# Optimization experiments

Measured on AMD Instinct MI355X. Metric: run time of the kernel, lower is better.

The kernel has to match this reference:

```python
import jax, jax.numpy as jnp
import numpy as np

NT, C, B, N, H, E = 32768, 128, 64, 512, 4, 524288  # total nodes, channels, graphs, nodes/graph, heads, edges
DH = C // H
EPS = 1e-5


def batchnorm(x, g, b):
    # BatchNorm1d over the node dimension (training-mode batch statistics)
    m = x.mean(axis=0)
    v = x.var(axis=0)
    return (x - m) * jax.lax.rsqrt(v + EPS) * g + b


def setup_inputs() -> dict:
    key = jax.random.key(0)
    ks = jax.random.split(key, 8)
    s = 1.0 / np.sqrt(C)
    return dict(
        x=jax.random.normal(ks[0], (NT, C), jnp.float32),
        edge_index=jax.random.randint(ks[1], (2, E), 0, NT, dtype=jnp.int32),
        Wc=jax.random.normal(ks[2], (C, C), jnp.float32) * s,
        bc=jnp.zeros((C,), jnp.float32),
        in_proj_w=jax.random.normal(ks[3], (3 * C, C), jnp.float32) * s,
        in_proj_b=jnp.zeros((3 * C,), jnp.float32),
        out_proj_w=jax.random.normal(ks[4], (C, C), jnp.float32) * s,
        out_proj_b=jnp.zeros((C,), jnp.float32),
        gn1=jnp.ones((C,), jnp.float32), bn1=jnp.zeros((C,), jnp.float32),
        gn2=jnp.ones((C,), jnp.float32), bn2=jnp.zeros((C,), jnp.float32),
        gn3=jnp.ones((C,), jnp.float32), bn3=jnp.zeros((C,), jnp.float32),
        Wm1=jax.random.normal(ks[5], (2 * C, C), jnp.float32) * s,
        bm1=jnp.zeros((2 * C,), jnp.float32),
        Wm2=jax.random.normal(ks[6], (C, 2 * C), jnp.float32) / np.sqrt(2 * C),
        bm2=jnp.zeros((C,), jnp.float32),
    )


def reference(x, edge_index, Wc, bc, in_proj_w, in_proj_b, out_proj_w, out_proj_b,
              gn1, bn1, gn2, bn2, gn3, bn3, Wm1, bm1, Wm2, bm2):
    # --- local branch: mean-aggregation message passing + linear + residual + BN ---
    src, dst = edge_index[0], edge_index[1]
    agg = jax.ops.segment_sum(x[src], dst, num_segments=NT)            # [NT, C]
    cnt = jax.ops.segment_sum(jnp.ones((E, 1), x.dtype), dst, num_segments=NT)
    agg = agg / jnp.maximum(cnt, 1.0)
    h_local = agg @ Wc.T + bc + x                                       # dropout p=0 -> no-op
    h_local = batchnorm(h_local, gn1, bn1)

    # --- global branch: to_dense_batch (equal-size graphs -> reshape) + MHA ---
    hd = x.reshape(B, N, C)
    qkv = hd @ in_proj_w.T + in_proj_b                                  # [B, N, 3C]
    q, k, v = jnp.split(qkv, 3, axis=-1)
    q = q.reshape(B, N, H, DH).transpose(0, 2, 1, 3)                    # [B, H, N, DH]
    k = k.reshape(B, N, H, DH).transpose(0, 2, 1, 3)
    v = v.reshape(B, N, H, DH).transpose(0, 2, 1, 3)
    scores = jnp.einsum('bhqd,bhkd->bhqk', q, k) / np.sqrt(DH)          # [B, H, N, N]
    attn = jax.nn.softmax(scores, axis=-1)
    o = jnp.einsum('bhqk,bhkd->bhqd', attn, v)                          # [B, H, N, DH]
    o = o.transpose(0, 2, 1, 3).reshape(B, N, C)
    h_attn = (o @ out_proj_w.T + out_proj_b).reshape(NT, C) + x
    h_attn = batchnorm(h_attn, gn2, bn2)

    # --- combine + MLP + final norm ---
    out = h_local + h_attn
    out = out + (jax.nn.relu(out @ Wm1.T + bm1) @ Wm2.T + bm2)
    return batchnorm(out, gn3, bn3)
```

## Files before the change

### kernel.cpp

```cpp
#include <hip/hip_runtime.h>
#include <cstddef>

#define NT    32768
#define CCH   128
#define BB    64
#define NNODE 512
#define NHEAD 4
#define DHEAD 32
#define EE    524288
#define EPS   1e-5f
#define MAXDEG 96

typedef unsigned short u16;
typedef unsigned int   u32;
typedef __attribute__((ext_vector_type(8))) short short8;
typedef __attribute__((ext_vector_type(4))) short short4v;
typedef __attribute__((ext_vector_type(4))) float f32x4;

__device__ __forceinline__ float b2f(u32 w) { return __uint_as_float(w << 16); }
__device__ __forceinline__ u16 f2b(float f) {
    u32 u = __float_as_uint(f);
    u += 0x7FFF + ((u >> 16) & 1);
    return (u16)(u >> 16);
}

__global__ __launch_bounds__(256) void prep_kernel(const float* __restrict__ x,
                                                   const float* __restrict__ Wc,
                                                   const float* __restrict__ Wqkv,
                                                   const float* __restrict__ Wo,
                                                   const float* __restrict__ Wm1,
                                                   const float* __restrict__ Wm2,
                                                   u16* __restrict__ xb,
                                                   u16* __restrict__ Wcb,
                                                   u16* __restrict__ Wqkvb,
                                                   u16* __restrict__ Wob,
                                                   u16* __restrict__ Wm1b,
                                                   u16* __restrict__ Wm2b,
                                                   const int* __restrict__ ei,
                                                   int* __restrict__ cursor,
                                                   int* __restrict__ bucket) {
    if (blockIdx.x >= 2120) {
        int e = (blockIdx.x - 2120) * 256 + threadIdx.x;
        int src = ei[e];
        int dst = ei[EE + e];
        int pos = atomicAdd(cursor + dst, 1);
        if (pos < MAXDEG) bucket[dst * MAXDEG + pos] = src;
        return;
    }
    int r = blockIdx.x * 256 + threadIdx.x;
    const float* src; u16* dst;
    if (r < 524288) { src = x; dst = xb; }
    else if ((r -= 524288) < 2048) { src = Wc; dst = Wcb; }
    else if ((r -= 2048) < 6144) { src = Wqkv; dst = Wqkvb; }
    else if ((r -= 6144) < 2048) { src = Wo; dst = Wob; }
    else if ((r -= 2048) < 4096) { src = Wm1; dst = Wm1b; }
    else { r -= 4096; src = Wm2; dst = Wm2b; }
    size_t base = (size_t)r * 8;
    float4 a = *(const float4*)(src + base);
    float4 b = *(const float4*)(src + base + 4);
    uint4 u;
    u.x = (u32)f2b(a.x) | ((u32)f2b(a.y) << 16);
    u.y = (u32)f2b(a.z) | ((u32)f2b(a.w) << 16);
    u.z = (u32)f2b(b.x) | ((u32)f2b(b.y) << 16);
    u.w = (u32)f2b(b.z) | ((u32)f2b(b.w) << 16);
    *(uint4*)(dst + base) = u;
}

__global__ __launch_bounds__(256) void aggregate(const int* __restrict__ bucket,
                                                 const int* __restrict__ cursor,
                                                 const u16* __restrict__ xb,
                                                 u16* __restrict__ agg) {
    int ln = threadIdx.x >> 5;
    int c4 = threadIdx.x & 31;
    int n = blockIdx.x * 8 + ln;
    __shared__ int srcs[8][MAXDEG];
    int d = min(cursor[n], MAXDEG);
    for (int j = c4; j < d; j += 32) srcs[ln][j] = bucket[n * MAXDEG + j];
    __syncthreads();
    float s0 = 0.f, s1 = 0.f, s2 = 0.f, s3 = 0.f;
    for (int j = 0; j < d; ++j) {
        uint2 w = *(const uint2*)(xb + (size_t)srcs[ln][j] * CCH + c4 * 4);
        s0 += b2f(w.x & 0xffffu);
        s1 += b2f(w.x >> 16);
        s2 += b2f(w.y & 0xffffu);
        s3 += b2f(w.y >> 16);
    }
    float inv = 1.0f / fmaxf((float)d, 1.0f);
    uint2 out;
    out.x = (u32)f2b(s0 * inv) | ((u32)f2b(s1 * inv) << 16);
    out.y = (u32)f2b(s2 * inv) | ((u32)f2b(s3 * inv) << 16);
    *(uint2*)(agg + (size_t)n * CCH + c4 * 4) = out;
}

template <bool RELU, int RESID, bool STATS>
__global__ __launch_bounds__(256) void gemm_mfma(const u16* __restrict__ A,
                                                 const u16* __restrict__ W,
                                                 const float* __restrict__ bias,
                                                 const u16* __restrict__ residb,
                                                 u16* __restrict__ outb,
                                                 float* __restrict__ sum,
                                                 float* __restrict__ sumsq,
                                                 int M, int N, int K) {
    __shared__ u16 As[128 * 32];
    __shared__ u16 Bs[128 * 32];
    __shared__ u16 Cs[4][16 * 72];
    __shared__ float csum[128];
    __shared__ float csq[128];
    int m0 = blockIdx.x * 128, n0 = blockIdx.y * 128;
    int tid = threadIdx.x;
    int lane = tid & 63, wave = tid >> 6;
    int wm = (wave & 1) * 64, wn = (wave >> 1) * 64;
    int l15 = lane & 15, l4 = lane >> 4;

    if (STATS) {
        if (tid < 128) { csum[tid] = 0.f; csq[tid] = 0.f; }
    }

    f32x4 zero = {0.f, 0.f, 0.f, 0.f};
    f32x4 acc[4][4];
#pragma unroll
    for (int i = 0; i < 4; ++i)
#pragma unroll
        for (int j = 0; j < 4; ++j) acc[i][j] = zero;

    int srow = tid >> 2;
    int scol = (tid & 3) * 8;

    int kIter = K >> 5;
    uint4 a0 = *(const uint4*)(A + (size_t)(m0 + srow) * K + scol);
    uint4 a1 = *(const uint4*)(A + (size_t)(m0 + srow + 64) * K + scol);
    uint4 b0 = *(const uint4*)(W + (size_t)(n0 + srow) * K + scol);
    uint4 b1 = *(const uint4*)(W + (size_t)(n0 + srow + 64) * K + scol);
    for (int ki = 0; ki < kIter; ++ki) {
        if (ki) __syncthreads();
        *(uint4*)&As[srow * 32 + scol] = a0;
        *(uint4*)&As[(srow + 64) * 32 + scol] = a1;
        *(uint4*)&Bs[srow * 32 + scol] = b0;
        *(uint4*)&Bs[(srow + 64) * 32 + scol] = b1;
        if (ki + 1 < kIter) {
            int k0 = (ki + 1) * 32;
            a0 = *(const uint4*)(A + (size_t)(m0 + srow) * K + k0 + scol);
            a1 = *(const uint4*)(A + (size_t)(m0 + srow + 64) * K + k0 + scol);
            b0 = *(const uint4*)(W + (size_t)(n0 + srow) * K + k0 + scol);
            b1 = *(const uint4*)(W + (size_t)(n0 + srow + 64) * K + k0 + scol);
        }
        __syncthreads();
        short8 af[4], bf[4];
#pragma unroll
        for (int t = 0; t < 4; ++t) {
            af[t] = *(const short8*)&As[(wm + t * 16 + l15) * 32 + l4 * 8];
            bf[t] = *(const short8*)&Bs[(wn + t * 16 + l15) * 32 + l4 * 8];
        }
#pragma unroll
        for (int mt = 0; mt < 4; ++mt)
#pragma unroll
            for (int nt = 0; nt < 4; ++nt)
                acc[mt][nt] = __builtin_amdgcn_mfma_f32_16x16x32_bf16(af[mt], bf[nt], acc[mt][nt], 0, 0, 0);
    }

    float ps[4] = {0.f, 0.f, 0.f, 0.f};
    float pq[4] = {0.f, 0.f, 0.f, 0.f};
    int rl = lane >> 3;
    int cg = lane & 7;
#pragma unroll
    for (int mt = 0; mt < 4; ++mt) {
#pragma unroll
        for (int nt = 0; nt < 4; ++nt) {
            int col = n0 + wn + nt * 16 + l15;
            float bs = bias[col];
#pragma unroll
            for (int r = 0; r < 4; ++r) {
                int row = m0 + wm + mt * 16 + l4 * 4 + r;
                float v = acc[mt][nt][r] + bs;
                if (RESID == 2) v += b2f(residb[(size_t)row * N + col]);
                if (RELU) v = fmaxf(v, 0.0f);
                Cs[wave][(l4 * 4 + r) * 72 + nt * 16 + l15] = f2b(v);
                if (STATS) { ps[nt] += v; pq[nt] += v * v; }
            }
        }
#pragma unroll
        for (int p = 0; p < 2; ++p) {
            int lrow = p * 8 + rl;
            uint4 wv = *(const uint4*)&Cs[wave][lrow * 72 + cg * 8];
            int grow = m0 + wm + mt * 16 + lrow;
            *(uint4*)(outb + (size_t)grow * N + n0 + wn + cg * 8) = wv;
        }
    }
    if (STATS) {
#pragma unroll
        for (int nt = 0; nt < 4; ++nt) {
            atomicAdd(&csum[wn + nt * 16 + l15], ps[nt]);
            atomicAdd(&csq[wn + nt * 16 + l15], pq[nt]);
        }
        __syncthreads();
        if (tid < 128) {
            atomicAdd(sum + n0 + tid, csum[tid]);
            atomicAdd(sumsq + n0 + tid, csq[tid]);
        }
    }
}

__global__ __launch_bounds__(256) void gemm_wc_qkv(const u16* __restrict__ aggb,
                                                   const u16* __restrict__ Wcb,
                                                   const float* __restrict__ bc,
                                                   const u16* __restrict__ xb,
                                                   u16* __restrict__ hlocb,
                                                   float* __restrict__ sum1,
                                                   float* __restrict__ sq1,
                                                   const u16* __restrict__ Wqkvb,
                                                   const float* __restrict__ bqkv,
                                                   u16* __restrict__ qkvb) {
    __shared__ u16 As[128 * 32];
    __shared__ u16 Bs[128 * 32];
    __shared__ u16 Cs[4][16 * 72];
    __shared__ float csum[128];
    __shared__ float csq[128];
    int y = blockIdx.y;
    bool wc = (y == 0);
    const u16* A = wc ? aggb : xb;
    const u16* W = wc ? Wcb : (Wqkvb + (size_t)(y - 1) * 128 * 128);
    const float* bias = wc ? bc : (bqkv + (y - 1) * 128);
    int ostride = wc ? 128 : 384;
    int ocol0 = wc ? 0 : (y - 1) * 128;
    u16* outp = wc ? hlocb : qkvb;

    int m0 = blockIdx.x * 128;
    int tid = threadIdx.x;
    int lane = tid & 63, wave = tid >> 6;
    int wm = (wave & 1) * 64, wn = (wave >> 1) * 64;
    int l15 = lane & 15, l4 = lane >> 4;

    if (wc && tid < 128) { csum[tid] = 0.f; csq[tid] = 0.f; }

    f32x4 zero = {0.f, 0.f, 0.f, 0.f};
    f32x4 acc[4][4];
#pragma unroll
    for (int i = 0; i < 4; ++i)
#pragma unroll
        for (int j = 0; j < 4; ++j) acc[i][j] = zero;

    int srow = tid >> 2;
    int scol = (tid & 3) * 8;

    uint4 a0 = *(const uint4*)(A + (size_t)(m0 + srow) * 128 + scol);
    uint4 a1 = *(const uint4*)(A + (size_t)(m0 + srow + 64) * 128 + scol);
    uint4 b0 = *(const uint4*)(W + (size_t)srow * 128 + scol);
    uint4 b1 = *(const uint4*)(W + (size_t)(srow + 64) * 128 + scol);
    for (int ki = 0; ki < 4; ++ki) {
        if (ki) __syncthreads();
        *(uint4*)&As[srow * 32 + scol] = a0;
        *(uint4*)&As[(srow + 64) * 32 + scol] = a1;
        *(uint4*)&Bs[srow * 32 + scol] = b0;
        *(uint4*)&Bs[(srow + 64) * 32 + scol] = b1;
        if (ki < 3) {
            int k0 = (ki + 1) * 32;
            a0 = *(const uint4*)(A + (size_t)(m0 + srow) * 128 + k0 + scol);
            a1 = *(const uint4*)(A + (size_t)(m0 + srow + 64) * 128 + k0 + scol);
            b0 = *(const uint4*)(W + (size_t)srow * 128 + k0 + scol);
            b1 = *(const uint4*)(W + (size_t)(srow + 64) * 128 + k0 + scol);
        }
        __syncthreads();
        short8 af[4], bf[4];
#pragma unroll
        for (int t = 0; t < 4; ++t) {
            af[t] = *(const short8*)&As[(wm + t * 16 + l15) * 32 + l4 * 8];
            bf[t] = *(const short8*)&Bs[(wn + t * 16 + l15) * 32 + l4 * 8];
        }
#pragma unroll
        for (int mt = 0; mt < 4; ++mt)
#pragma unroll
            for (int nt = 0; nt < 4; ++nt)
                acc[mt][nt] = __builtin_amdgcn_mfma_f32_16x16x32_bf16(af[mt], bf[nt], acc[mt][nt], 0, 0, 0);
    }

    float ps[4] = {0.f, 0.f, 0.f, 0.f};
    float pq[4] = {0.f, 0.f, 0.f, 0.f};
    int rl = lane >> 3;
    int cg = lane & 7;
#pragma unroll
    for (int mt = 0; mt < 4; ++mt) {
#pragma unroll
        for (int nt = 0; nt < 4; ++nt) {
            int lcol = wn + nt * 16 + l15;
            float bs = bias[lcol];
#pragma unroll
            for (int r = 0; r < 4; ++r) {
                int row = m0 + wm + mt * 16 + l4 * 4 + r;
                float v = acc[mt][nt][r] + bs;
                if (wc) v += b2f(xb[(size_t)row * 128 + lcol]);
                Cs[wave][(l4 * 4 + r) * 72 + nt * 16 + l15] = f2b(v);
                if (wc) { ps[nt] += v; pq[nt] += v * v; }
            }
        }
#pragma unroll
        for (int p = 0; p < 2; ++p) {
            int lrow = p * 8 + rl;
            uint4 wv = *(const uint4*)&Cs[wave][lrow * 72 + cg * 8];
            int grow = m0 + wm + mt * 16 + lrow;
            *(uint4*)(outp + (size_t)grow * ostride + ocol0 + wn + cg * 8) = wv;
        }
    }
    if (wc) {
#pragma unroll
        for (int nt = 0; nt < 4; ++nt) {
            atomicAdd(&csum[wn + nt * 16 + l15], ps[nt]);
            atomicAdd(&csq[wn + nt * 16 + l15], pq[nt]);
        }
        __syncthreads();
        if (tid < 128) {
            atomicAdd(sum1 + tid, csum[tid]);
            atomicAdd(sq1 + tid, csq[tid]);
        }
    }
}

__global__ __launch_bounds__(256) void gemm_m1c(const u16* __restrict__ hlocb,
                                                const u16* __restrict__ t2b,
                                                const float* __restrict__ sum1,
                                                const float* __restrict__ sq1,
                                                const float* __restrict__ g1,
                                                const float* __restrict__ bt1,
                                                const float* __restrict__ sum2,
                                                const float* __restrict__ sq2,
                                                const float* __restrict__ g2,
                                                const float* __restrict__ bt2,
                                                u16* __restrict__ shb,
                                                const u16* __restrict__ Wm1b,
                                                const float* __restrict__ bm1,
                                                u16* __restrict__ hidb) {
    __shared__ u16 As[128 * 32];
    __shared__ u16 Bs[128 * 32];
    __shared__ u16 Cs[4][16 * 72];
    __shared__ float AF1[128], BF1[128], AF2[128], BF2[128];
    int tid = threadIdx.x;
    {
        int c = tid & 127;
        const float* sm = (tid < 128) ? sum1 : sum2;
        const float* sq = (tid < 128) ? sq1 : sq2;
        const float* g  = (tid < 128) ? g1 : g2;
        const float* bt = (tid < 128) ? bt1 : bt2;
        float m = sm[c] * (1.0f / NT);
        float v = sq[c] * (1.0f / NT) - m * m;
        float a = g[c] * rsqrtf(v + EPS);
        if (tid < 128) { AF1[c] = a; BF1[c] = bt[c] - m * a; }
        else           { AF2[c] = a; BF2[c] = bt[c] - m * a; }
    }
    int m0 = blockIdx.x * 128, n0 = blockIdx.y * 128;
    int lane = tid & 63, wave = tid >> 6;
    int wm = (wave & 1) * 64, wn = (wave >> 1) * 64;
    int l15 = lane & 15, l4 = lane >> 4;

    f32x4 zero = {0.f, 0.f, 0.f, 0.f};
    f32x4 acc[4][4];
#pragma unroll
    for (int i = 0; i < 4; ++i)
#pragma unroll
        for (int j = 0; j < 4; ++j) acc[i][j] = zero;

    int srow = tid >> 2;
    int scol = (tid & 3) * 8;
    bool wr = (blockIdx.y == 0);

    uint4 h0 = *(const uint4*)(hlocb + (size_t)(m0 + srow) * 128 + scol);
    uint4 h1 = *(const uint4*)(hlocb + (size_t)(m0 + srow + 64) * 128 + scol);
    uint4 t0 = *(const uint4*)(t2b + (size_t)(m0 + srow) * 128 + scol);
    uint4 t1 = *(const uint4*)(t2b + (size_t)(m0 + srow + 64) * 128 + scol);
    uint4 b0 = *(const uint4*)(Wm1b + (size_t)(n0 + srow) * 128 + scol);
    uint4 b1 = *(const uint4*)(Wm1b + (size_t)(n0 + srow + 64) * 128 + scol);
    __syncthreads();
    for (int ki = 0; ki < 4; ++ki) {
        int k0 = ki * 32;
        if (ki) __syncthreads();
        uint4 c0, c1;
        {
            const u32 hw[4] = {h0.x, h0.y, h0.z, h0.w};
            const u32 tw[4] = {t0.x, t0.y, t0.z, t0.w};
            u32 ow[4];
#pragma unroll
            for (int p = 0; p < 4; ++p) {
                int cc = k0 + scol + p * 2;
                float v0 = AF1[cc] * b2f(hw[p] & 0xffffu) + BF1[cc] + AF2[cc] * b2f(tw[p] & 0xffffu) + BF2[cc];
                float v1 = AF1[cc + 1] * b2f(hw[p] >> 16) + BF1[cc + 1] + AF2[cc + 1] * b2f(tw[p] >> 16) + BF2[cc + 1];
                ow[p] = (u32)f2b(v0) | ((u32)f2b(v1) << 16);
            }
            c0.x = ow[0]; c0.y = ow[1]; c0.z = ow[2]; c0.w = ow[3];
        }
        {
            const u32 hw[4] = {h1.x, h1.y, h1.z, h1.w};
            const u32 tw[4] = {t1.x, t1.y, t1.z, t1.w};
            u32 ow[4];
#pragma unroll
            for (int p = 0; p < 4; ++p) {
                int cc = k0 + scol + p * 2;
                float v0 = AF1[cc] * b2f(hw[p] & 0xffffu) + BF1[cc] + AF2[cc] * b2f(tw[p] & 0xffffu) + BF2[cc];
                float v1 = AF1[cc + 1] * b2f(hw[p] >> 16) + BF1[cc + 1] + AF2[cc + 1] * b2f(tw[p] >> 16) + BF2[cc + 1];
                ow[p] = (u32)f2b(v0) | ((u32)f2b(v1) << 16);
            }
            c1.x = ow[0]; c1.y = ow[1]; c1.z = ow[2]; c1.w = ow[3];
        }
        *(uint4*)&As[srow * 32 + scol] = c0;
        *(uint4*)&As[(srow + 64) * 32 + scol] = c1;
        *(uint4*)&Bs[srow * 32 + scol] = b0;
        *(uint4*)&Bs[(srow + 64) * 32 + scol] = b1;
        if (wr) {
            *(uint4*)(shb + (size_t)(m0 + srow) * 128 + k0 + scol) = c0;
            *(uint4*)(shb + (size_t)(m0 + srow + 64) * 128 + k0 + scol) = c1;
        }
        if (ki < 3) {
            int kn = k0 + 32;
            h0 = *(const uint4*)(hlocb + (size_t)(m0 + srow) * 128 + kn + scol);
            h1 = *(const uint4*)(hlocb + (size_t)(m0 + srow + 64) * 128 + kn + scol);
            t0 = *(const uint4*)(t2b + (size_t)(m0 + srow) * 128 + kn + scol);
            t1 = *(const uint4*)(t2b + (size_t)(m0 + srow + 64) * 128 + kn + scol);
            b0 = *(const uint4*)(Wm1b + (size_t)(n0 + srow) * 128 + kn + scol);
            b1 = *(const uint4*)(Wm1b + (size_t)(n0 + srow + 64) * 128 + kn + scol);
        }
        __syncthreads();
        short8 af[4], bf[4];
#pragma unroll
        for (int t = 0; t < 4; ++t) {
            af[t] = *(const short8*)&As[(wm + t * 16 + l15) * 32 + l4 * 8];
            bf[t] = *(const short8*)&Bs[(wn + t * 16 + l15) * 32 + l4 * 8];
        }
#pragma unroll
        for (int mt = 0; mt < 4; ++mt)
#pragma unroll
            for (int nt = 0; nt < 4; ++nt)
                acc[mt][nt] = __builtin_amdgcn_mfma_f32_16x16x32_bf16(af[mt], bf[nt], acc[mt][nt], 0, 0, 0);
    }

    int rl = lane >> 3;
    int cg = lane & 7;
#pragma unroll
    for (int mt = 0; mt < 4; ++mt) {
#pragma unroll
        for (int nt = 0; nt < 4; ++nt) {
            int col = n0 + wn + nt * 16 + l15;
            float bs = bm1[col];
#pragma unroll
            for (int r = 0; r < 4; ++r) {
                float v = fmaxf(acc[mt][nt][r] + bs, 0.0f);
                Cs[wave][(l4 * 4 + r) * 72 + nt * 16 + l15] = f2b(v);
            }
        }
#pragma unroll
        for (int p = 0; p < 2; ++p) {
            int lrow = p * 8 + rl;
            uint4 wv = *(const uint4*)&Cs[wave][lrow * 72 + cg * 8];
            int grow = m0 + wm + mt * 16 + lrow;
            *(uint4*)(hidb + (size_t)grow * 256 + n0 + wn + cg * 8) = wv;
        }
    }
}

__global__ __launch_bounds__(256) void final_bn(const u16* __restrict__ X,
                                                const float* __restrict__ sum3,
                                                const float* __restrict__ sq3,
                                                const float* __restrict__ g3,
                                                const float* __restrict__ bt3,
                                                float* __restrict__ outp) {
    __shared__ float A3[128], B3[128];
    int t = threadIdx.x;
    if (t < 128) {
        float m = sum3[t] * (1.0f / NT);
        float v = sq3[t] * (1.0f / NT) - m * m;
        float a = g3[t] * rsqrtf(v + EPS);
        A3[t] = a;
        B3[t] = bt3[t] - m * a;
    }
    __syncthreads();
    int i8 = blockIdx.x * 256 + t;
    size_t i = (size_t)i8 * 8;
    int c = (int)(i & (CCH - 1));
    uint4 u = *(const uint4*)(X + i);
    float x[8];
    x[0] = b2f(u.x & 0xffffu); x[1] = b2f(u.x >> 16);
    x[2] = b2f(u.y & 0xffffu); x[3] = b2f(u.y >> 16);
    x[4] = b2f(u.z & 0xffffu); x[5] = b2f(u.z >> 16);
    x[6] = b2f(u.w & 0xffffu); x[7] = b2f(u.w >> 16);
    float4 o0, o1;
    o0.x = A3[c + 0] * x[0] + B3[c + 0];
    o0.y = A3[c + 1] * x[1] + B3[c + 1];
    o0.z = A3[c + 2] * x[2] + B3[c + 2];
    o0.w = A3[c + 3] * x[3] + B3[c + 3];
    o1.x = A3[c + 4] * x[4] + B3[c + 4];
    o1.y = A3[c + 5] * x[5] + B3[c + 5];
    o1.z = A3[c + 6] * x[6] + B3[c + 6];
    o1.w = A3[c + 7] * x[7] + B3[c + 7];
    *(float4*)(outp + i) = o0;
    *(float4*)(outp + i + 4) = o1;
}

__global__ __launch_bounds__(512) void attn_mfma(const u16* __restrict__ qkv,
                                                 u16* __restrict__ o) {
    __shared__ __align__(16) u16 Ks[512 * 40];
    __shared__ __align__(16) u16 Vt[32 * 520];
    int bh = blockIdx.x;
    int b = bh >> 2, h = bh & 3;
    int tid = threadIdx.x;
    int lane = tid & 63, wave = tid >> 6;
    int quad = lane >> 4, l15 = lane & 15;
    const float scale = 0.1767766952966369f;

    const u16* kvbase = qkv + (size_t)b * 512 * 384 + 128 + h * 32;
    for (int idx = tid; idx < 2048; idx += 512) {
        int row = idx >> 2, c = idx & 3;
        *(uint4*)&Ks[row * 40 + c * 8] = *(const uint4*)(kvbase + (size_t)row * 384 + c * 8);
    }
    for (int idx = tid; idx < 2048; idx += 512) {
        int row = idx >> 2, c = idx & 3;
        uint4 u = *(const uint4*)(kvbase + 128 + (size_t)row * 384 + c * 8);
        u16 e[8];
        *(uint4*)e = u;
#pragma unroll
        for (int i = 0; i < 8; ++i) Vt[(c * 8 + i) * 520 + row] = e[i];
    }
    __syncthreads();

    f32x4 zero = {0.f, 0.f, 0.f, 0.f};
    for (int qt = 0; qt < 4; ++qt) {
        int qbase = wave * 64 + qt * 16;
        short8 qf = *(const short8*)(qkv + (size_t)(b * 512 + qbase + l15) * 384 + h * 32 + quad * 8);
        float lq = 0.f;
        f32x4 oa[2] = {zero, zero};

        for (int kv0 = 0; kv0 < 512; kv0 += 64) {
            f32x4 s[4];
#pragma unroll
            for (int t = 0; t < 4; ++t) {
                short8 kb = *(const short8*)&Ks[(kv0 + t * 16 + l15) * 40 + quad * 8];
                s[t] = __builtin_amdgcn_mfma_f32_16x16x32_bf16(kb, qf, zero, 0, 0, 0);
            }
            short8 pa[4];
#pragma unroll
            for (int t = 0; t < 4; ++t) {
                float p0 = __expf(s[t][0] * scale);
                float p1 = __expf(s[t][1] * scale);
                float p2 = __expf(s[t][2] * scale);
                float p3 = __expf(s[t][3] * scale);
                lq += (p0 + p1) + (p2 + p3);
                short8 a8 = {(short)f2b(p0), (short)f2b(p1), (short)f2b(p2), (short)f2b(p3), 0, 0, 0, 0};
                pa[t] = a8;
            }
#pragma unroll
            for (int t = 0; t < 4; ++t) {
                int tbase = kv0 + t * 16;
#pragma unroll
                for (int n = 0; n < 2; ++n) {
                    short4v v4 = *(const short4v*)&Vt[(n * 16 + l15) * 520 + tbase + quad * 4];
                    short8 vb = {v4.x, v4.y, v4.z, v4.w, 0, 0, 0, 0};
                    oa[n] = __builtin_amdgcn_mfma_f32_16x16x32_bf16(pa[t], vb, oa[n], 0, 0, 0);
                }
            }
        }
        lq += __shfl_xor(lq, 16);
        lq += __shfl_xor(lq, 32);
        u16* op = o + (size_t)(b * 512 + qbase) * 128 + h * 32;
#pragma unroll
        for (int r = 0; r < 4; ++r) {
            float Lr = __shfl(lq, quad * 4 + r);
            float inv = 1.0f / Lr;
#pragma unroll
            for (int n = 0; n < 2; ++n)
                op[(quad * 4 + r) * 128 + n * 16 + l15] = f2b(oa[n][r] * inv);
        }
    }
}

extern "C" void kernel_launch(void* const* d_in, const int* in_sizes, int n_in,
                              void* d_out, int out_size, void* d_ws, size_t ws_size,
                              hipStream_t stream) {
    const float* x    = (const float*)d_in[0];
    const int*   ei   = (const int*)d_in[1];
    const float* Wc   = (const float*)d_in[2];
    const float* bc   = (const float*)d_in[3];
    const float* Wqkv = (const float*)d_in[4];
    const float* bqkv = (const float*)d_in[5];
    const float* Wo   = (const float*)d_in[6];
    const float* bo   = (const float*)d_in[7];
    const float* gn1  = (const float*)d_in[8];
    const float* bn1b = (const float*)d_in[9];
    const float* gn2  = (const float*)d_in[10];
    const float* bn2b = (const float*)d_in[11];
    const float* gn3  = (const float*)d_in[12];
    const float* bn3b = (const float*)d_in[13];
    const float* Wm1  = (const float*)d_in[14];
    const float* bm1  = (const float*)d_in[15];
    const float* Wm2  = (const float*)d_in[16];
    const float* bm2  = (const float*)d_in[17];
    float* outp = (float*)d_out;

    char* w = (char*)d_ws;
    const size_t MB = 1024 * 1024;
    u16* xb    = (u16*)(w);
    u16* hlocb = (u16*)(w + 8 * MB);
    u16* t2b   = (u16*)(w + 16 * MB);
    u16* out2b = (u16*)(w + 24 * MB);
    u16* qkvb  = (u16*)(w + 32 * MB);
    u16* hidb  = (u16*)(w + 56 * MB);
    u16* shb   = (u16*)(w + 72 * MB);
    int* bucket = (int*)(w + 80 * MB);
    int* cursor = (int*)(w + 92 * MB);
    float* stats = (float*)(w + 92 * MB + 128 * 1024);
    u16* Wcb   = (u16*)(w + 93 * MB);
    u16* Wqkvb = Wcb + 16384;
    u16* Wob   = Wqkvb + 49152;
    u16* Wm1b  = Wob + 16384;
    u16* Wm2b  = Wm1b + 32768;
    float* sum1 = stats;        float* sq1 = stats + 128;
    float* sum2 = stats + 256;  float* sq2 = stats + 384;
    float* sum3 = stats + 512;  float* sq3 = stats + 640;

    hipMemsetAsync(cursor, 0, 128 * 1024 + 6 * 128 * 4, stream);

    prep_kernel<<<2120 + 2048, 256, 0, stream>>>(x, Wc, Wqkv, Wo, Wm1, Wm2,
                                                 xb, Wcb, Wqkvb, Wob, Wm1b, Wm2b,
                                                 ei, cursor, bucket);

    aggregate<<<NT / 8, 256, 0, stream>>>(bucket, cursor, xb, shb);

    {
        dim3 g(NT / 128, 4);
        gemm_wc_qkv<<<g, 256, 0, stream>>>(shb, Wcb, bc, xb, hlocb, sum1, sq1,
                                           Wqkvb, bqkv, qkvb);
    }

    attn_mfma<<<BB * NHEAD, 512, 0, stream>>>(qkvb, shb);

    {
        dim3 g(NT / 128, 1);
        gemm_mfma<false, 2, true><<<g, 256, 0, stream>>>(
            shb, Wob, bo, xb, t2b, sum2, sq2, NT, 128, 128);
    }

    {
        dim3 g(NT / 128, 2);
        gemm_m1c<<<g, 256, 0, stream>>>(hlocb, t2b, sum1, sq1, gn1, bn1b,
                                        sum2, sq2, gn2, bn2b, shb, Wm1b, bm1, hidb);
    }

    {
        dim3 g(NT / 128, 1);
        gemm_mfma<false, 2, true><<<g, 256, 0, stream>>>(
            hidb, Wm2b, bm2, shb, out2b, sum3, sq3, NT, 128, 256);
    }

    final_bn<<<NT * CCH / 8 / 256, 256, 0, stream>>>(out2b, sum3, sq3, gn3, bn3b, outp);
}
```

Measured before the change: 249.0 us.

## Co-schedule independent stages in merged kernels to fill the GPU

Reschedules the pipeline so independent work shares a launch. The aggregation and the QKV projection now run as disjoint block ranges of one kernel, and the attention and the Wc GEMM with its BN stats run as block ranges of a second kernel. The attention blocks drop from 512 to 256 threads with 8 query tiles per wave, and attention output moves to a separate buffer. The goal is to fill idle CUs (attention alone had only 256 blocks) and remove a launch, at the cost of a larger shared-memory footprint and possible load imbalance between the heavy attention blocks and the short GEMM blocks.

```diff
diff --git a/kernel.cpp b/kernel.cpp
--- a/kernel.cpp
+++ b/kernel.cpp
@@ -66,30 +66,289 @@
     *(uint4*)(dst + base) = u;
 }
 
-__global__ __launch_bounds__(256) void aggregate(const int* __restrict__ bucket,
-                                                 const int* __restrict__ cursor,
-                                                 const u16* __restrict__ xb,
-                                                 u16* __restrict__ agg) {
-    int ln = threadIdx.x >> 5;
-    int c4 = threadIdx.x & 31;
-    int n = blockIdx.x * 8 + ln;
-    __shared__ int srcs[8][MAXDEG];
-    int d = min(cursor[n], MAXDEG);
-    for (int j = c4; j < d; j += 32) srcs[ln][j] = bucket[n * MAXDEG + j];
+__global__ __launch_bounds__(256) void stage2_kernel(const int* __restrict__ bucket,
+                                                     const int* __restrict__ cursor,
+                                                     const u16* __restrict__ xb,
+                                                     u16* __restrict__ aggb,
+                                                     const u16* __restrict__ Wqkvb,
+                                                     const float* __restrict__ bqkv,
+                                                     u16* __restrict__ qkvb) {
+    __shared__ __align__(16) char smem[26624];
+    int tid = threadIdx.x;
+    if (blockIdx.x < 4096) {
+        int* srcs = (int*)smem;
+        int ln = tid >> 5;
+        int c4 = tid & 31;
+        int n = blockIdx.x * 8 + ln;
+        int d = min(cursor[n], MAXDEG);
+        for (int j = c4; j < d; j += 32) srcs[ln * MAXDEG + j] = bucket[n * MAXDEG + j];
+        __syncthreads();
+        float s0 = 0.f, s1 = 0.f, s2 = 0.f, s3 = 0.f;
+        for (int j = 0; j < d; ++j) {
+            uint2 w = *(const uint2*)(xb + (size_t)srcs[ln * MAXDEG + j] * CCH + c4 * 4);
+            s0 += b2f(w.x & 0xffffu);
+            s1 += b2f(w.x >> 16);
+            s2 += b2f(w.y & 0xffffu);
+            s3 += b2f(w.y >> 16);
+        }
+        float inv = 1.0f / fmaxf((float)d, 1.0f);
+        uint2 out;
+        out.x = (u32)f2b(s0 * inv) | ((u32)f2b(s1 * inv) << 16);
+        out.y = (u32)f2b(s2 * inv) | ((u32)f2b(s3 * inv) << 16);
+        *(uint2*)(aggb + (size_t)n * CCH + c4 * 4) = out;
+        return;
+    }
+    int bx = blockIdx.x - 4096;
+    int y = bx >> 8;
+    int m0 = (bx & 255) * 128;
+    const u16* W = Wqkvb + (size_t)y * 128 * 128;
+    const float* bias = bqkv + y * 128;
+    u16* As = (u16*)smem;
+    u16* Bs = (u16*)(smem + 8192);
+    u16* Cs = (u16*)(smem + 16384);
+
+    int lane = tid & 63, wave = tid >> 6;
+    int wm = (wave & 1) * 64, wn = (wave >> 1) * 64;
+    int l15 = lane & 15, l4 = lane >> 4;
+
+    f32x4 zero = {0.f, 0.f, 0.f, 0.f};
+    f32x4 acc[4][4];
+#pragma unroll
+    for (int i = 0; i < 4; ++i)
+#pragma unroll
+        for (int j = 0; j < 4; ++j) acc[i][j] = zero;
+
+    int srow = tid >> 2;
+    int scol = (tid & 3) * 8;
+
+    uint4 a0 = *(const uint4*)(xb + (size_t)(m0 + srow) * 128 + scol);
+    uint4 a1 = *(const uint4*)(xb + (size_t)(m0 + srow + 64) * 128 + scol);
+    uint4 b0 = *(const uint4*)(W + (size_t)srow * 128 + scol);
+    uint4 b1 = *(const uint4*)(W + (size_t)(srow + 64) * 128 + scol);
+    for (int ki = 0; ki < 4; ++ki) {
+        if (ki) __syncthreads();
+        *(uint4*)&As[srow * 32 + scol] = a0;
+        *(uint4*)&As[(srow + 64) * 32 + scol] = a1;
+        *(uint4*)&Bs[srow * 32 + scol] = b0;
+        *(uint4*)&Bs[(srow + 64) * 32 + scol] = b1;
+        if (ki < 3) {
+            int k0 = (ki + 1) * 32;
+            a0 = *(const uint4*)(xb + (size_t)(m0 + srow) * 128 + k0 + scol);
+            a1 = *(const uint4*)(xb + (size_t)(m0 + srow + 64) * 128 + k0 + scol);
+            b0 = *(const uint4*)(W + (size_t)srow * 128 + k0 + scol);
+            b1 = *(const uint4*)(W + (size_t)(srow + 64) * 128 + k0 + scol);
+        }
+        __syncthreads();
+        short8 af[4], bf[4];
+#pragma unroll
+        for (int t = 0; t < 4; ++t) {
+            af[t] = *(const short8*)&As[(wm + t * 16 + l15) * 32 + l4 * 8];
+            bf[t] = *(const short8*)&Bs[(wn + t * 16 + l15) * 32 + l4 * 8];
+        }
+#pragma unroll
+        for (int mt = 0; mt < 4; ++mt)
+#pragma unroll
+            for (int nt = 0; nt < 4; ++nt)
+                acc[mt][nt] = __builtin_amdgcn_mfma_f32_16x16x32_bf16(af[mt], bf[nt], acc[mt][nt], 0, 0, 0);
+    }
+
+    int rl = lane >> 3;
+    int cg = lane & 7;
+    u16* Cw = Cs + wave * 16 * 72;
+#pragma unroll
+    for (int mt = 0; mt < 4; ++mt) {
+#pragma unroll
+        for (int nt = 0; nt < 4; ++nt) {
+            float bs = bias[wn + nt * 16 + l15];
+#pragma unroll
+            for (int r = 0; r < 4; ++r)
+                Cw[(l4 * 4 + r) * 72 + nt * 16 + l15] = f2b(acc[mt][nt][r] + bs);
+        }
+#pragma unroll
+        for (int p = 0; p < 2; ++p) {
+            int lrow = p * 8 + rl;
+            uint4 wv = *(const uint4*)&Cw[lrow * 72 + cg * 8];
+            int grow = m0 + wm + mt * 16 + lrow;
+            *(uint4*)(qkvb + (size_t)grow * 384 + y * 128 + wn + cg * 8) = wv;
+        }
+    }
+}
+
+__global__ __launch_bounds__(256) void stage3_kernel(const u16* __restrict__ qkvb,
+                                                     u16* __restrict__ ob,
+                                                     const u16* __restrict__ aggb,
+                                                     const u16* __restrict__ Wcb,
+                                                     const float* __restrict__ bc,
+                                                     const u16* __restrict__ xb,
+                                                     u16* __restrict__ hlocb,
+                                                     float* __restrict__ sum1,
+                                                     float* __restrict__ sq1) {
+    __shared__ __align__(16) char smem[74240];
+    int tid = threadIdx.x;
+    int lane = tid & 63, wave = tid >> 6;
+    int quad = lane >> 4, l15 = lane & 15, l4 = lane >> 4;
+
+    if (blockIdx.x < 256) {
+        u16* Ks = (u16*)smem;
+        u16* Vt = (u16*)(smem + 40960);
+        int bh = blockIdx.x;
+        int b = bh >> 2, h = bh & 3;
+        const float scale = 0.1767766952966369f;
+
+        const u16* kvbase = qkvb + (size_t)b * 512 * 384 + 128 + h * 32;
+        for (int idx = tid; idx < 2048; idx += 256) {
+            int row = idx >> 2, c = idx & 3;
+            *(uint4*)&Ks[row * 40 + c * 8] = *(const uint4*)(kvbase + (size_t)row * 384 + c * 8);
+        }
+        for (int idx = tid; idx < 2048; idx += 256) {
+            int row = idx >> 2, c = idx & 3;
+            uint4 u = *(const uint4*)(kvbase + 128 + (size_t)row * 384 + c * 8);
+            u16 e[8];
+            *(uint4*)e = u;
+#pragma unroll
+            for (int i = 0; i < 8; ++i) Vt[(c * 8 + i) * 520 + row] = e[i];
+        }
+        __syncthreads();
+
+        f32x4 zero = {0.f, 0.f, 0.f, 0.f};
+        for (int qt = 0; qt < 8; ++qt) {
+            int qbase = wave * 128 + qt * 16;
+            short8 qf = *(const short8*)(qkvb + (size_t)(b * 512 + qbase + l15) * 384 + h * 32 + quad * 8);
+            float lq = 0.f;
+            f32x4 oa[2] = {zero, zero};
+
+            for (int kv0 = 0; kv0 < 512; kv0 += 64) {
+                f32x4 s[4];
+#pragma unroll
+                for (int t = 0; t < 4; ++t) {
+                    short8 kb = *(const short8*)&Ks[(kv0 + t * 16 + l15) * 40 + quad * 8];
+                    s[t] = __builtin_amdgcn_mfma_f32_16x16x32_bf16(kb, qf, zero, 0, 0, 0);
+                }
+                short8 pa[4];
+#pragma unroll
+                for (int t = 0; t < 4; ++t) {
+                    float p0 = __expf(s[t][0] * scale);
+                    float p1 = __expf(s[t][1] * scale);
+                    float p2 = __expf(s[t][2] * scale);
+                    float p3 = __expf(s[t][3] * scale);
+                    lq += (p0 + p1) + (p2 + p3);
+                    short8 a8 = {(short)f2b(p0), (short)f2b(p1), (short)f2b(p2), (short)f2b(p3), 0, 0, 0, 0};
+                    pa[t] = a8;
+                }
+#pragma unroll
+                for (int t = 0; t < 4; ++t) {
+                    int tbase = kv0 + t * 16;
+#pragma unroll
+                    for (int n = 0; n < 2; ++n) {
+                        short4v v4 = *(const short4v*)&Vt[(n * 16 + l15) * 520 + tbase + quad * 4];
+                        short8 vb = {v4.x, v4.y, v4.z, v4.w, 0, 0, 0, 0};
+                        oa[n] = __builtin_amdgcn_mfma_f32_16x16x32_bf16(pa[t], vb, oa[n], 0, 0, 0);
+                    }
+                }
+            }
+            lq += __shfl_xor(lq, 16);
+            lq += __shfl_xor(lq, 32);
+            u16* op = ob + (size_t)(b * 512 + qbase) * 128 + h * 32;
+#pragma unroll
+            for (int r = 0; r < 4; ++r) {
+                float Lr = __shfl(lq, quad * 4 + r);
+                float inv = 1.0f / Lr;
+#pragma unroll
+                for (int n = 0; n < 2; ++n)
+                    op[(quad * 4 + r) * 128 + n * 16 + l15] = f2b(oa[n][r] * inv);
+            }
+        }
+        return;
+    }
+
+    int m0 = (blockIdx.x - 256) * 128;
+    u16* As = (u16*)smem;
+    u16* Bs = (u16*)(smem + 8192);
+    u16* Cs = (u16*)(smem + 16384);
+    float* csum = (float*)(smem + 25600);
+    float* csq  = (float*)(smem + 26112);
+    int wm = (wave & 1) * 64, wn = (wave >> 1) * 64;
+
+    if (tid < 128) { csum[tid] = 0.f; csq[tid] = 0.f; }
+
+    f32x4 zero = {0.f, 0.f, 0.f, 0.f};
+    f32x4 acc[4][4];
+#pragma unroll
+    for (int i = 0; i < 4; ++i)
+#pragma unroll
+        for (int j = 0; j < 4; ++j) acc[i][j] = zero;
+
+    int srow = tid >> 2;
+    int scol = (tid & 3) * 8;
+
+    uint4 a0 = *(const uint4*)(aggb + (size_t)(m0 + srow) * 128 + scol);
+    uint4 a1 = *(const uint4*)(aggb + (size_t)(m0 + srow + 64) * 128 + scol);
+    uint4 b0 = *(const uint4*)(Wcb + (size_t)srow * 128 + scol);
+    uint4 b1 = *(const uint4*)(Wcb + (size_t)(srow + 64) * 128 + scol);
+    for (int ki = 0; ki < 4; ++ki) {
+        if (ki) __syncthreads();
+        *(uint4*)&As[srow * 32 + scol] = a0;
+        *(uint4*)&As[(srow + 64) * 32 + scol] = a1;
+        *(uint4*)&Bs[srow * 32 + scol] = b0;
+        *(uint4*)&Bs[(srow + 64) * 32 + scol] = b1;
+        if (ki < 3) {
+            int k0 = (ki + 1) * 32;
+            a0 = *(const uint4*)(aggb + (size_t)(m0 + srow) * 128 + k0 + scol);
+            a1 = *(const uint4*)(aggb + (size_t)(m0 + srow + 64) * 128 + k0 + scol);
+            b0 = *(const uint4*)(Wcb + (size_t)srow * 128 + k0 + scol);
+            b1 = *(const uint4*)(Wcb + (size_t)(srow + 64) * 128 + k0 + scol);
+        }
+        __syncthreads();
+        short8 af[4], bf[4];
+#pragma unroll
+        for (int t = 0; t < 4; ++t) {
+            af[t] = *(const short8*)&As[(wm + t * 16 + l15) * 32 + l4 * 8];
+            bf[t] = *(const short8*)&Bs[(wn + t * 16 + l15) * 32 + l4 * 8];
+        }
+#pragma unroll
+        for (int mt = 0; mt < 4; ++mt)
+#pragma unroll
+            for (int nt = 0; nt < 4; ++nt)
+                acc[mt][nt] = __builtin_amdgcn_mfma_f32_16x16x32_bf16(af[mt], bf[nt], acc[mt][nt], 0, 0, 0);
+    }
+
+    float ps[4] = {0.f, 0.f, 0.f, 0.f};
+    float pq[4] = {0.f, 0.f, 0.f, 0.f};
+    int rl = lane >> 3;
+    int cg = lane & 7;
+    u16* Cw = Cs + wave * 16 * 72;
+#pragma unroll
+    for (int mt = 0; mt < 4; ++mt) {
+#pragma unroll
+        for (int nt = 0; nt < 4; ++nt) {
+            int lcol = wn + nt * 16 + l15;
+            float bs = bc[lcol];
+#pragma unroll
+            for (int r = 0; r < 4; ++r) {
+                int row = m0 + wm + mt * 16 + l4 * 4 + r;
+                float v = acc[mt][nt][r] + bs + b2f(xb[(size_t)row * 128 + lcol]);
+                Cw[(l4 * 4 + r) * 72 + nt * 16 + l15] = f2b(v);
+                ps[nt] += v; pq[nt] += v * v;
+            }
+        }
+#pragma unroll
+        for (int p = 0; p < 2; ++p) {
+            int lrow = p * 8 + rl;
+            uint4 wv = *(const uint4*)&Cw[lrow * 72 + cg * 8];
+            int grow = m0 + wm + mt * 16 + lrow;
+            *(uint4*)(hlocb + (size_t)grow * 128 + wn + cg * 8) = wv;
+        }
+    }
+#pragma unroll
+    for (int nt = 0; nt < 4; ++nt) {
+        atomicAdd(&csum[wn + nt * 16 + l15], ps[nt]);
+        atomicAdd(&csq[wn + nt * 16 + l15], pq[nt]);
+    }
     __syncthreads();
-    float s0 = 0.f, s1 = 0.f, s2 = 0.f, s3 = 0.f;
-    for (int j = 0; j < d; ++j) {
-        uint2 w = *(const uint2*)(xb + (size_t)srcs[ln][j] * CCH + c4 * 4);
-        s0 += b2f(w.x & 0xffffu);
-        s1 += b2f(w.x >> 16);
-        s2 += b2f(w.y & 0xffffu);
-        s3 += b2f(w.y >> 16);
-    }
-    float inv = 1.0f / fmaxf((float)d, 1.0f);
-    uint2 out;
-    out.x = (u32)f2b(s0 * inv) | ((u32)f2b(s1 * inv) << 16);
-    out.y = (u32)f2b(s2 * inv) | ((u32)f2b(s3 * inv) << 16);
-    *(uint2*)(agg + (size_t)n * CCH + c4 * 4) = out;
+    if (tid < 128) {
+        atomicAdd(sum1 + tid, csum[tid]);
+        atomicAdd(sq1 + tid, csq[tid]);
+    }
 }
 
 template <bool RELU, int RESID, bool STATS>
@@ -196,120 +455,6 @@
         if (tid < 128) {
             atomicAdd(sum + n0 + tid, csum[tid]);
             atomicAdd(sumsq + n0 + tid, csq[tid]);
-        }
-    }
-}
-
-__global__ __launch_bounds__(256) void gemm_wc_qkv(const u16* __restrict__ aggb,
-                                                   const u16* __restrict__ Wcb,
-                                                   const float* __restrict__ bc,
-                                                   const u16* __restrict__ xb,
-                                                   u16* __restrict__ hlocb,
-                                                   float* __restrict__ sum1,
-                                                   float* __restrict__ sq1,
-                                                   const u16* __restrict__ Wqkvb,
-                                                   const float* __restrict__ bqkv,
-                                                   u16* __restrict__ qkvb) {
-    __shared__ u16 As[128 * 32];
-    __shared__ u16 Bs[128 * 32];
-    __shared__ u16 Cs[4][16 * 72];
-    __shared__ float csum[128];
-    __shared__ float csq[128];
-    int y = blockIdx.y;
-    bool wc = (y == 0);
-    const u16* A = wc ? aggb : xb;
-    const u16* W = wc ? Wcb : (Wqkvb + (size_t)(y - 1) * 128 * 128);
-    const float* bias = wc ? bc : (bqkv + (y - 1) * 128);
-    int ostride = wc ? 128 : 384;
-    int ocol0 = wc ? 0 : (y - 1) * 128;
-    u16* outp = wc ? hlocb : qkvb;
-
-    int m0 = blockIdx.x * 128;
-    int tid = threadIdx.x;
-    int lane = tid & 63, wave = tid >> 6;
-    int wm = (wave & 1) * 64, wn = (wave >> 1) * 64;
-    int l15 = lane & 15, l4 = lane >> 4;
-
-    if (wc && tid < 128) { csum[tid] = 0.f; csq[tid] = 0.f; }
-
-    f32x4 zero = {0.f, 0.f, 0.f, 0.f};
-    f32x4 acc[4][4];
-#pragma unroll
-    for (int i = 0; i < 4; ++i)
-#pragma unroll
-        for (int j = 0; j < 4; ++j) acc[i][j] = zero;
-
-    int srow = tid >> 2;
-    int scol = (tid & 3) * 8;
-
-    uint4 a0 = *(const uint4*)(A + (size_t)(m0 + srow) * 128 + scol);
-    uint4 a1 = *(const uint4*)(A + (size_t)(m0 + srow + 64) * 128 + scol);
-    uint4 b0 = *(const uint4*)(W + (size_t)srow * 128 + scol);
-    uint4 b1 = *(const uint4*)(W + (size_t)(srow + 64) * 128 + scol);
-    for (int ki = 0; ki < 4; ++ki) {
-        if (ki) __syncthreads();
-        *(uint4*)&As[srow * 32 + scol] = a0;
-        *(uint4*)&As[(srow + 64) * 32 + scol] = a1;
-        *(uint4*)&Bs[srow * 32 + scol] = b0;
-        *(uint4*)&Bs[(srow + 64) * 32 + scol] = b1;
-        if (ki < 3) {
-            int k0 = (ki + 1) * 32;
-            a0 = *(const uint4*)(A + (size_t)(m0 + srow) * 128 + k0 + scol);
-            a1 = *(const uint4*)(A + (size_t)(m0 + srow + 64) * 128 + k0 + scol);
-            b0 = *(const uint4*)(W + (size_t)srow * 128 + k0 + scol);
-            b1 = *(const uint4*)(W + (size_t)(srow + 64) * 128 + k0 + scol);
-        }
-        __syncthreads();
-        short8 af[4], bf[4];
-#pragma unroll
-        for (int t = 0; t < 4; ++t) {
-            af[t] = *(const short8*)&As[(wm + t * 16 + l15) * 32 + l4 * 8];
-            bf[t] = *(const short8*)&Bs[(wn + t * 16 + l15) * 32 + l4 * 8];
-        }
-#pragma unroll
-        for (int mt = 0; mt < 4; ++mt)
-#pragma unroll
-            for (int nt = 0; nt < 4; ++nt)
-                acc[mt][nt] = __builtin_amdgcn_mfma_f32_16x16x32_bf16(af[mt], bf[nt], acc[mt][nt], 0, 0, 0);
-    }
-
-    float ps[4] = {0.f, 0.f, 0.f, 0.f};
-    float pq[4] = {0.f, 0.f, 0.f, 0.f};
-    int rl = lane >> 3;
-    int cg = lane & 7;
-#pragma unroll
-    for (int mt = 0; mt < 4; ++mt) {
-#pragma unroll
-        for (int nt = 0; nt < 4; ++nt) {
-            int lcol = wn + nt * 16 + l15;
-            float bs = bias[lcol];
-#pragma unroll
-            for (int r = 0; r < 4; ++r) {
-                int row = m0 + wm + mt * 16 + l4 * 4 + r;
-                float v = acc[mt][nt][r] + bs;
-                if (wc) v += b2f(xb[(size_t)row * 128 + lcol]);
-                Cs[wave][(l4 * 4 + r) * 72 + nt * 16 + l15] = f2b(v);
-                if (wc) { ps[nt] += v; pq[nt] += v * v; }
-            }
-        }
-#pragma unroll
-        for (int p = 0; p < 2; ++p) {
-            int lrow = p * 8 + rl;
-            uint4 wv = *(const uint4*)&Cs[wave][lrow * 72 + cg * 8];
-            int grow = m0 + wm + mt * 16 + lrow;
-            *(uint4*)(outp + (size_t)grow * ostride + ocol0 + wn + cg * 8) = wv;
-        }
-    }
-    if (wc) {
-#pragma unroll
-        for (int nt = 0; nt < 4; ++nt) {
-            atomicAdd(&csum[wn + nt * 16 + l15], ps[nt]);
-            atomicAdd(&csq[wn + nt * 16 + l15], pq[nt]);
-        }
-        __syncthreads();
-        if (tid < 128) {
-            atomicAdd(sum1 + tid, csum[tid]);
-            atomicAdd(sq1 + tid, csq[tid]);
         }
     }
 }
@@ -491,82 +636,6 @@
     *(float4*)(outp + i + 4) = o1;
 }
 
-__global__ __launch_bounds__(512) void attn_mfma(const u16* __restrict__ qkv,
-                                                 u16* __restrict__ o) {
-    __shared__ __align__(16) u16 Ks[512 * 40];
-    __shared__ __align__(16) u16 Vt[32 * 520];
-    int bh = blockIdx.x;
-    int b = bh >> 2, h = bh & 3;
-    int tid = threadIdx.x;
-    int lane = tid & 63, wave = tid >> 6;
-    int quad = lane >> 4, l15 = lane & 15;
-    const float scale = 0.1767766952966369f;
-
-    const u16* kvbase = qkv + (size_t)b * 512 * 384 + 128 + h * 32;
-    for (int idx = tid; idx < 2048; idx += 512) {
-        int row = idx >> 2, c = idx & 3;
-        *(uint4*)&Ks[row * 40 + c * 8] = *(const uint4*)(kvbase + (size_t)row * 384 + c * 8);
-    }
-    for (int idx = tid; idx < 2048; idx += 512) {
-        int row = idx >> 2, c = idx & 3;
-        uint4 u = *(const uint4*)(kvbase + 128 + (size_t)row * 384 + c * 8);
-        u16 e[8];
-        *(uint4*)e = u;
-#pragma unroll
-        for (int i = 0; i < 8; ++i) Vt[(c * 8 + i) * 520 + row] = e[i];
-    }
-    __syncthreads();
-
-    f32x4 zero = {0.f, 0.f, 0.f, 0.f};
-    for (int qt = 0; qt < 4; ++qt) {
-        int qbase = wave * 64 + qt * 16;
-        short8 qf = *(const short8*)(qkv + (size_t)(b * 512 + qbase + l15) * 384 + h * 32 + quad * 8);
-        float lq = 0.f;
-        f32x4 oa[2] = {zero, zero};
-
-        for (int kv0 = 0; kv0 < 512; kv0 += 64) {
-            f32x4 s[4];
-#pragma unroll
-            for (int t = 0; t < 4; ++t) {
-                short8 kb = *(const short8*)&Ks[(kv0 + t * 16 + l15) * 40 + quad * 8];
-                s[t] = __builtin_amdgcn_mfma_f32_16x16x32_bf16(kb, qf, zero, 0, 0, 0);
-            }
-            short8 pa[4];
-#pragma unroll
-            for (int t = 0; t < 4; ++t) {
-                float p0 = __expf(s[t][0] * scale);
-                float p1 = __expf(s[t][1] * scale);
-                float p2 = __expf(s[t][2] * scale);
-                float p3 = __expf(s[t][3] * scale);
-                lq += (p0 + p1) + (p2 + p3);
-                short8 a8 = {(short)f2b(p0), (short)f2b(p1), (short)f2b(p2), (short)f2b(p3), 0, 0, 0, 0};
-                pa[t] = a8;
-            }
-#pragma unroll
-            for (int t = 0; t < 4; ++t) {
-                int tbase = kv0 + t * 16;
-#pragma unroll
-                for (int n = 0; n < 2; ++n) {
-                    short4v v4 = *(const short4v*)&Vt[(n * 16 + l15) * 520 + tbase + quad * 4];
-                    short8 vb = {v4.x, v4.y, v4.z, v4.w, 0, 0, 0, 0};
-                    oa[n] = __builtin_amdgcn_mfma_f32_16x16x32_bf16(pa[t], vb, oa[n], 0, 0, 0);
-                }
-            }
-        }
-        lq += __shfl_xor(lq, 16);
-        lq += __shfl_xor(lq, 32);
-        u16* op = o + (size_t)(b * 512 + qbase) * 128 + h * 32;
-#pragma unroll
-        for (int r = 0; r < 4; ++r) {
-            float Lr = __shfl(lq, quad * 4 + r);
-            float inv = 1.0f / Lr;
-#pragma unroll
-            for (int n = 0; n < 2; ++n)
-                op[(quad * 4 + r) * 128 + n * 16 + l15] = f2b(oa[n][r] * inv);
-        }
-    }
-}
-
 extern "C" void kernel_launch(void* const* d_in, const int* in_sizes, int n_in,
                               void* d_out, int out_size, void* d_ws, size_t ws_size,
                               hipStream_t stream) {
@@ -607,6 +676,7 @@
     u16* Wob   = Wqkvb + 49152;
     u16* Wm1b  = Wob + 16384;
     u16* Wm2b  = Wm1b + 32768;
+    u16* ob    = (u16*)(w + 94 * MB);
     float* sum1 = stats;        float* sq1 = stats + 128;
     float* sum2 = stats + 256;  float* sq2 = stats + 384;
     float* sum3 = stats + 512;  float* sq3 = stats + 640;
@@ -617,20 +687,16 @@
                                                  xb, Wcb, Wqkvb, Wob, Wm1b, Wm2b,
                                                  ei, cursor, bucket);
 
-    aggregate<<<NT / 8, 256, 0, stream>>>(bucket, cursor, xb, shb);
-
-    {
-        dim3 g(NT / 128, 4);
-        gemm_wc_qkv<<<g, 256, 0, stream>>>(shb, Wcb, bc, xb, hlocb, sum1, sq1,
-                                           Wqkvb, bqkv, qkvb);
-    }
-
-    attn_mfma<<<BB * NHEAD, 512, 0, stream>>>(qkvb, shb);
+    stage2_kernel<<<4096 + 768, 256, 0, stream>>>(bucket, cursor, xb, shb,
+                                                  Wqkvb, bqkv, qkvb);
+
+    stage3_kernel<<<512, 256, 0, stream>>>(qkvb, ob, shb, Wcb, bc, xb,
+                                           hlocb, sum1, sq1);
 
     {
         dim3 g(NT / 128, 1);
         gemm_mfma<false, 2, true><<<g, 256, 0, stream>>>(
-            shb, Wob, bo, xb, t2b, sum2, sq2, NT, 128, 128);
+            ob, Wob, bo, xb, t2b, sum2, sq2, NT, 128, 128);
     }
 
     {
```

Measured after the change: 257.5 us. +3.4%, slower.
